# Kernel optimization log

Hardware: AMD Instinct MI355X
Metric: run time of the kernel (lower is better)

## Reference

```python
import jax, jax.numpy as jnp
import numpy as np

B, H0, W0, C = 16, 56, 56, 96
NH, WS, SS = 3, 7, 3
HID, NCL, TAU = 384, 128, 0.5
EPS = 1e-6

def layernorm(x, g, b):
    m = jnp.mean(x, -1, keepdims=True)
    v = jnp.mean((x - m) ** 2, -1, keepdims=True)
    return (x - m) * jax.lax.rsqrt(v + 1e-5) * g + b

def setup_inputs() -> dict:
    key = jax.random.key(0)
    ks = jax.random.split(key, 16)
    s = lambda d: 1.0 / np.sqrt(d)
    return {
        "x": jax.random.normal(ks[0], (B, H0 * W0, C), jnp.float32),
        "norm1_g": jnp.ones((C,)), "norm1_b": jnp.zeros((C,)),
        "qkv_w": jax.random.normal(ks[1], (3 * C, C)) * s(C),
        "qkv_b": jnp.zeros((3 * C,)),
        "proj_w": jax.random.normal(ks[2], (C, C)) * s(C),
        "proj_b": jnp.zeros((C,)),
        "norm2_g": jnp.ones((C,)), "norm2_b": jnp.zeros((C,)),
        "ffn_norm_g": jnp.ones((C,)), "ffn_norm_b": jnp.zeros((C,)),
        "pin_w": jax.random.normal(ks[3], (HID, C)) * s(C),
        "pin_b": jnp.zeros((HID,)),
        "tm_inc": jax.random.normal(ks[4], (NCL, 2 * HID)) * 0.5,
        "tm_out": jax.random.normal(ks[5], (NCL, C)) * s(NCL),
        "gate": jnp.float32(0.5),
        "H": H0, "W": W0,
    }

def window_attention(win, qkv_w, qkv_b, proj_w, proj_b):
    N, T, Cc = win.shape
    hd = Cc // NH
    qkv = win @ qkv_w.T + qkv_b                      # [N, T, 3C]
    qkv = qkv.reshape(N, T, 3, NH, hd).transpose(2, 0, 3, 1, 4)
    q, k, v = qkv[0], qkv[1], qkv[2]                 # [N, nh, T, hd]
    attn = jax.nn.softmax(jnp.einsum('nhqd,nhkd->nhqk', q, k) * (hd ** -0.5), axis=-1)
    out = jnp.einsum('nhqk,nhkd->nhqd', attn, v).transpose(0, 2, 1, 3).reshape(N, T, Cc)
    return out @ proj_w.T + proj_b

def tm_ffn(x, ffn_norm_g, ffn_norm_b, pin_w, pin_b, tm_inc, tm_out, gate):
    # x: [B, T, C]
    Bb, T, Cc = x.shape
    y = jax.nn.sigmoid(layernorm(x, ffn_norm_g, ffn_norm_b) @ pin_w.T + pin_b)  # [B,T,HID]
    flat = y.reshape(Bb * T, HID)
    lits = jnp.clip(jnp.concatenate([flat, 1.0 - flat], axis=-1), EPS, 1.0)     # [N, 2*HID]
    m = jax.nn.sigmoid(tm_inc)
    hard = (m > TAU).astype(m.dtype)
    m_ste = m + jax.lax.stop_gradient(hard - m)      # binary via STE
    # binary mask -> conjunction prod_k l_k^{m_jk} = exp(log(l) @ m^T)
    clauses = jnp.exp(jnp.log(lits) @ m_ste.T)       # [N, NCL]
    logits = (clauses @ tm_out).reshape(Bb, T, Cc)
    g = jax.nn.sigmoid(gate)
    return g * logits + (1.0 - g) * jax.nn.sigmoid(logits)

def reference(x, norm1_g, norm1_b, qkv_w, qkv_b, proj_w, proj_b,
              norm2_g, norm2_b, ffn_norm_g, ffn_norm_b,
              pin_w, pin_b, tm_inc, tm_out, gate, H, W):
    Bb, L, Cc = x.shape
    shortcut = x
    y = layernorm(x, norm1_g, norm1_b).reshape(Bb, H, W, Cc)
    pad_h = (WS - H % WS) % WS
    pad_w = (WS - W % WS) % WS
    if pad_h or pad_w:
        y = jnp.pad(y, ((0, 0), (0, pad_h), (0, pad_w), (0, 0)))
    Hp, Wp = y.shape[1], y.shape[2]
    if SS > 0:
        y = jnp.roll(y, shift=(-SS, -SS), axis=(1, 2))
    # window partition
    y = y.reshape(Bb, Hp // WS, WS, Wp // WS, WS, Cc).transpose(0, 1, 3, 2, 4, 5)
    win = y.reshape(-1, WS * WS, Cc)
    a = window_attention(win, qkv_w, qkv_b, proj_w, proj_b)
    a = a.reshape(Bb, Hp // WS, Wp // WS, WS, WS, Cc)
    if SS > 0:
        a = jnp.roll(a, shift=(SS, SS), axis=(3, 4))
    # window reverse
    a = a.transpose(0, 1, 3, 2, 4, 5).reshape(Bb, Hp, Wp, Cc)
    if pad_h or pad_w:
        a = a[:, :H, :W, :]
    a = a.reshape(Bb, H * W, Cc)
    x1 = shortcut + a
    x2 = x1 + tm_ffn(layernorm(x1, norm2_g, norm2_b),
                     ffn_norm_g, ffn_norm_b, pin_w, pin_b, tm_inc, tm_out, gate)
    return x2
```

## Files before the change

kernel.cpp:

```cpp
#include <hip/hip_runtime.h>

#define NB 16
#define NHH 56
#define NWW 56
#define NC 96
#define NL (NHH*NWW)
#define NTOK (NB*NL)
#define WSZ 7
#define NT 49
#define SSH 3
#define NWIN 1024
#define HDIM 32
#define HID_ 384
#define NCL_ 128
#define NLIT 768
#define EPS_ 1e-6f
#define LOG_EPS -13.815510558f

typedef unsigned short u16;
typedef unsigned int   u32;
typedef __attribute__((ext_vector_type(8))) short short8;
typedef __attribute__((ext_vector_type(4))) float f32x4;

__device__ __forceinline__ float us2f(u16 u) {
  union { u32 u; float f; } x; x.u = ((u32)u) << 16; return x.f;
}
__device__ __forceinline__ u16 f2us(float f) {
  union { float f; u32 u; } x; x.f = f;
  u32 lsb = (x.u >> 16) & 1u;
  return (u16)((x.u + 0x7fffu + lsb) >> 16);
}
__device__ __forceinline__ float sigmoidf_(float x) { return 1.f / (1.f + __expf(-x)); }

__global__ __launch_bounds__(256) void k0_prep(const float* __restrict__ tm_inc,
                                               const float* __restrict__ pin_w,
                                               const float* __restrict__ tm_out,
                                               const float* __restrict__ qkv_w,
                                               const float* __restrict__ proj_w,
                                               u16* __restrict__ maskb,
                                               u16* __restrict__ pinwb,
                                               u16* __restrict__ tmoT,
                                               u16* __restrict__ qkvwb,
                                               u16* __restrict__ projwb) {
  int idx = blockIdx.x * 256 + threadIdx.x;
  if (idx < NCL_ * NLIT) {
    int c = idx / NLIT, q = idx - c * NLIT;
    int j = (q & 1) ? (q >> 1) + HID_ : (q >> 1);
    maskb[idx] = (tm_inc[(size_t)c * NLIT + j] > 0.f) ? (u16)0x3F80 : (u16)0;
  }
  if (idx < HID_ * NC)
    pinwb[idx] = f2us(pin_w[idx]);
  if (idx < NC * NCL_) {
    int c = idx / NCL_, k = idx - c * NCL_;
    tmoT[idx] = f2us(tm_out[(size_t)k * NC + c]);
  }
  if (idx < 3 * NC * NC)
    qkvwb[idx] = f2us(qkv_w[idx]);
  if (idx < NC * NC)
    projwb[idx] = f2us(proj_w[idx]);
}

__global__ __launch_bounds__(256, 4) void k2_attn(const float* __restrict__ x,
                                               const float* __restrict__ n1g,
                                               const float* __restrict__ n1b,
                                               const u16* __restrict__ qkvwb,
                                               const float* __restrict__ qkv_b,
                                               const u16* __restrict__ projwb,
                                               const float* __restrict__ proj_b,
                                               float* __restrict__ x1) {
  __shared__ __align__(16) u16 syb[64 * 104];
  __shared__ __align__(16) u16 sk [64 * 104];
  __shared__ __align__(16) u16 svT[96 * 72];
  const int tid  = threadIdx.x;
  const int wave = tid >> 6;
  const int lane = tid & 63;
  const int l16  = lane & 15;
  const int quad = lane >> 4;
  const int win  = blockIdx.x;
  const int t0   = wave * 16;
  const int bb = win >> 6, wl = win & 63;
  const int hbase = (wl >> 3) * WSZ, wbase = (wl & 7) * WSZ;

  {
    const int t = tid >> 2, s = tid & 3;
    if (t < NT) {
      int hp = hbase + t / WSZ, wp = wbase + t % WSZ;
      int h = hp + SSH; if (h >= NHH) h -= NHH;
      int w = wp + SSH; if (w >= NWW) w -= NWW;
      const float* xp = x + ((size_t)bb * NL + (size_t)h * NWW + w) * NC;
      float4 v[6];
      float sum = 0.f;
      #pragma unroll
      for (int k = 0; k < 6; ++k) {
        v[k] = *reinterpret_cast<const float4*>(xp + s * 4 + k * 16);
        sum += v[k].x + v[k].y + v[k].z + v[k].w;
      }
      sum += __shfl_xor(sum, 1); sum += __shfl_xor(sum, 2);
      float mean = sum * (1.f / 96.f);
      float ssq = 0.f;
      #pragma unroll
      for (int k = 0; k < 6; ++k) {
        float d0 = v[k].x - mean, d1 = v[k].y - mean;
        float d2 = v[k].z - mean, d3 = v[k].w - mean;
        ssq += d0 * d0 + d1 * d1 + d2 * d2 + d3 * d3;
      }
      ssq += __shfl_xor(ssq, 1); ssq += __shfl_xor(ssq, 2);
      float rstd = rsqrtf(ssq * (1.f / 96.f) + 1e-5f);
      #pragma unroll
      for (int k = 0; k < 6; ++k) {
        int c = s * 4 + k * 16;
        const float4 g4 = *reinterpret_cast<const float4*>(n1g + c);
        const float4 b4 = *reinterpret_cast<const float4*>(n1b + c);
        syb[t * 104 + c + 0] = f2us((v[k].x - mean) * rstd * g4.x + b4.x);
        syb[t * 104 + c + 1] = f2us((v[k].y - mean) * rstd * g4.y + b4.y);
        syb[t * 104 + c + 2] = f2us((v[k].z - mean) * rstd * g4.z + b4.z);
        syb[t * 104 + c + 3] = f2us((v[k].w - mean) * rstd * g4.w + b4.w);
      }
    } else {
      #pragma unroll
      for (int k = 0; k < 6; ++k) {
        int c = s * 4 + k * 16;
        syb[t * 104 + c + 0] = 0; syb[t * 104 + c + 1] = 0;
        syb[t * 104 + c + 2] = 0; syb[t * 104 + c + 3] = 0;
      }
    }
  }

  {
    short8 afr[3];
    #pragma unroll
    for (int ks = 0; ks < 3; ++ks)
      afr[ks] = *reinterpret_cast<const short8*>(&syb[(t0 + l16) * 104 + quad * 8 + ks * 32]);
    short8 rb[4][3];
    #pragma unroll
    for (int p = 0; p < 4; ++p)
      #pragma unroll
      for (int ks = 0; ks < 3; ++ks)
        rb[p][ks] = *reinterpret_cast<const short8*>(
            qkvwb + (size_t)(p * 16 + l16) * NC + quad * 8 + ks * 32);
    #pragma unroll
    for (int nt = 0; nt < 18; ++nt) {
      const int n0 = nt * 16;
      const float bias = qkv_b[n0 + l16];
      short8 b0 = rb[nt & 3][0], b1 = rb[nt & 3][1], b2 = rb[nt & 3][2];
      if (nt + 4 < 18) {
        #pragma unroll
        for (int ks = 0; ks < 3; ++ks)
          rb[nt & 3][ks] = *reinterpret_cast<const short8*>(
              qkvwb + (size_t)((nt + 4) * 16 + l16) * NC + quad * 8 + ks * 32);
      }
      f32x4 acc = {0.f, 0.f, 0.f, 0.f};
      acc = __builtin_amdgcn_mfma_f32_16x16x32_bf16(afr[0], b0, acc, 0, 0, 0);
      acc = __builtin_amdgcn_mfma_f32_16x16x32_bf16(afr[1], b1, acc, 0, 0, 0);
      acc = __builtin_amdgcn_mfma_f32_16x16x32_bf16(afr[2], b2, acc, 0, 0, 0);
      const int part = nt / 6;
      const int oc = n0 - part * 96 + l16;
      if (part < 2) {
        u16* dst = (part == 0) ? syb : sk;
        #pragma unroll
        for (int r = 0; r < 4; ++r)
          dst[(t0 + quad * 4 + r) * 104 + oc] = f2us(acc[r] + bias);
      } else {
        #pragma unroll
        for (int r = 0; r < 4; ++r)
          svT[oc * 72 + (t0 + quad * 4 + r)] = f2us(acc[r] + bias);
      }
    }
  }
  __syncthreads();

  u16* spw = sk + wave * 16 * 72;
  const float sscale = 0.17677669529663687f;
  short8 qf[3];
  f32x4 s[3][4];
  #pragma unroll
  for (int h = 0; h < 3; ++h)
    qf[h] = *reinterpret_cast<const short8*>(&syb[(t0 + l16) * 104 + h * HDIM + quad * 8]);
  #pragma unroll
  for (int h = 0; h < 3; ++h) {
    const int d0 = h * HDIM;
    #pragma unroll
    for (int nt = 0; nt < 4; ++nt) {
      short8 kf = *reinterpret_cast<const short8*>(&sk[(nt * 16 + l16) * 104 + d0 + quad * 8]);
      f32x4 a = {0.f, 0.f, 0.f, 0.f};
      s[h][nt] = __builtin_amdgcn_mfma_f32_16x16x32_bf16(qf[h], kf, a, 0, 0, 0);
    }
  }
  __syncthreads();
  #pragma unroll
  for (int h = 0; h < 3; ++h) {
    const int d0 = h * HDIM;
    #pragma unroll
    for (int nt = 0; nt < 4; ++nt)
      #pragma unroll
      for (int r = 0; r < 4; ++r) s[h][nt][r] *= sscale;
    if (l16 >= 1) {
      #pragma unroll
      for (int r = 0; r < 4; ++r) s[h][3][r] = -1e30f;
    }
    #pragma unroll
    for (int r = 0; r < 4; ++r) {
      float m = fmaxf(fmaxf(s[h][0][r], s[h][1][r]), fmaxf(s[h][2][r], s[h][3][r]));
      #pragma unroll
      for (int off = 8; off > 0; off >>= 1) m = fmaxf(m, __shfl_xor(m, off, 16));
      float e0 = __expf(s[h][0][r] - m), e1 = __expf(s[h][1][r] - m);
      float e2 = __expf(s[h][2][r] - m), e3 = __expf(s[h][3][r] - m);
      float sum = e0 + e1 + e2 + e3;
      #pragma unroll
      for (int off = 8; off > 0; off >>= 1) sum += __shfl_xor(sum, off, 16);
      float inv = 1.f / sum;
      const int row = quad * 4 + r;
      spw[row * 72 +      l16] = f2us(e0 * inv);
      spw[row * 72 + 16 + l16] = f2us(e1 * inv);
      spw[row * 72 + 32 + l16] = f2us(e2 * inv);
      spw[row * 72 + 48 + l16] = f2us(e3 * inv);
    }
    short8 pa[2];
    pa[0] = *reinterpret_cast<const short8*>(&spw[l16 * 72 + quad * 8]);
    pa[1] = *reinterpret_cast<const short8*>(&spw[l16 * 72 + 32 + quad * 8]);
    #pragma unroll
    for (int nt = 0; nt < 2; ++nt) {
      const int c0 = d0 + nt * 16;
      f32x4 acc = {0.f, 0.f, 0.f, 0.f};
      #pragma unroll
      for (int ks = 0; ks < 2; ++ks) {
        short8 vb = *reinterpret_cast<const short8*>(&svT[(c0 + l16) * 72 + ks * 32 + quad * 8]);
        acc = __builtin_amdgcn_mfma_f32_16x16x32_bf16(pa[ks], vb, acc, 0, 0, 0);
      }
      #pragma unroll
      for (int r = 0; r < 4; ++r)
        syb[(t0 + quad * 4 + r) * 104 + c0 + l16] = f2us(acc[r]);
    }
  }

  {
    short8 aa[3];
    #pragma unroll
    for (int ks = 0; ks < 3; ++ks)
      aa[ks] = *reinterpret_cast<const short8*>(&syb[(t0 + l16) * 104 + quad * 8 + ks * 32]);

    size_t tokr[4]; bool tval[4];
    #pragma unroll
    for (int r = 0; r < 4; ++r) {
      const int t = t0 + quad * 4 + r;
      tval[r] = (t < NT);
      int rr = t / WSZ + SSH; if (rr >= WSZ) rr -= WSZ;
      int qq = t % WSZ + SSH; if (qq >= WSZ) qq -= WSZ;
      tokr[r] = (size_t)bb * NL + (size_t)(hbase + rr) * NWW + (wbase + qq);
    }
    float xv[6][4];
    #pragma unroll
    for (int nt = 0; nt < 6; ++nt)
      #pragma unroll
      for (int r = 0; r < 4; ++r)
        xv[nt][r] = tval[r] ? x[tokr[r] * NC + nt * 16 + l16] : 0.f;

    short8 pbr[2][3];
    #pragma unroll
    for (int ks = 0; ks < 3; ++ks)
      pbr[0][ks] = *reinterpret_cast<const short8*>(
          projwb + (size_t)l16 * NC + quad * 8 + ks * 32);
    #pragma unroll
    for (int nt = 0; nt < 6; ++nt) {
      const int n0 = nt * 16;
      const float pb = proj_b[n0 + l16];
      short8 b0 = pbr[nt & 1][0], b1 = pbr[nt & 1][1], b2 = pbr[nt & 1][2];
      if (nt + 1 < 6) {
        #pragma unroll
        for (int ks = 0; ks < 3; ++ks)
          pbr[(nt + 1) & 1][ks] = *reinterpret_cast<const short8*>(
              projwb + (size_t)((nt + 1) * 16 + l16) * NC + quad * 8 + ks * 32);
      }
      f32x4 acc = {0.f, 0.f, 0.f, 0.f};
      acc = __builtin_amdgcn_mfma_f32_16x16x32_bf16(aa[0], b0, acc, 0, 0, 0);
      acc = __builtin_amdgcn_mfma_f32_16x16x32_bf16(aa[1], b1, acc, 0, 0, 0);
      acc = __builtin_amdgcn_mfma_f32_16x16x32_bf16(aa[2], b2, acc, 0, 0, 0);
      #pragma unroll
      for (int r = 0; r < 4; ++r) {
        if (tval[r])
          x1[tokr[r] * NC + n0 + l16] = xv[nt][r] + acc[r] + pb;
      }
    }
  }
}

__global__ __launch_bounds__(256, 6) void k4_ffn(const float* __restrict__ x1,
                                              const float* __restrict__ g2,
                                              const float* __restrict__ b2,
                                              const float* __restrict__ gf,
                                              const float* __restrict__ bf,
                                              const u16* __restrict__ pinwb,
                                              const float* __restrict__ pin_b,
                                              const u16* __restrict__ maskb,
                                              const u16* __restrict__ tmoT,
                                              const float* __restrict__ gate,
                                              float* __restrict__ out) {
  __shared__ __align__(16) u16 lit[16 * 776];
  u16* szb  = lit;
  u16* claT = lit;
  const int tid  = threadIdx.x;
  const int wave = tid >> 6;
  const int lane = tid & 63;
  const int l16  = lane & 15;
  const int quad = lane >> 4;
  const size_t tok0 = (size_t)blockIdx.x * 16;

  {
    const int t = tid >> 4, s = tid & 15;
    const float* xp = x1 + (tok0 + t) * NC;
    float2 v[3];
    float sum = 0.f;
    #pragma unroll
    for (int k = 0; k < 3; ++k) {
      const int c = s * 2 + k * 32;
      v[k] = *reinterpret_cast<const float2*>(xp + c);
      sum += v[k].x + v[k].y;
    }
    #pragma unroll
    for (int off = 8; off > 0; off >>= 1) sum += __shfl_xor(sum, off, 16);
    const float mean = sum * (1.f / 96.f);
    float ssq = 0.f;
    #pragma unroll
    for (int k = 0; k < 3; ++k) {
      float d0 = v[k].x - mean, d1 = v[k].y - mean;
      ssq += d0 * d0 + d1 * d1;
    }
    #pragma unroll
    for (int off = 8; off > 0; off >>= 1) ssq += __shfl_xor(ssq, off, 16);
    const float rstd = rsqrtf(ssq * (1.f / 96.f) + 1e-5f);
    float tv[6];
    float sum2 = 0.f;
    #pragma unroll
    for (int k = 0; k < 3; ++k) {
      const int c = s * 2 + k * 32;
      const float2 gg = *reinterpret_cast<const float2*>(g2 + c);
      const float2 bb = *reinterpret_cast<const float2*>(b2 + c);
      tv[2 * k]     = (v[k].x - mean) * rstd * gg.x + bb.x;
      tv[2 * k + 1] = (v[k].y - mean) * rstd * gg.y + bb.y;
      sum2 += tv[2 * k] + tv[2 * k + 1];
    }
    #pragma unroll
    for (int off = 8; off > 0; off >>= 1) sum2 += __shfl_xor(sum2, off, 16);
    const float mean2 = sum2 * (1.f / 96.f);
    float ssq2 = 0.f;
    #pragma unroll
    for (int k = 0; k < 3; ++k) {
      float d0 = tv[2 * k] - mean2, d1 = tv[2 * k + 1] - mean2;
      ssq2 += d0 * d0 + d1 * d1;
    }
    #pragma unroll
    for (int off = 8; off > 0; off >>= 1) ssq2 += __shfl_xor(ssq2, off, 16);
    const float rstd2 = rsqrtf(ssq2 * (1.f / 96.f) + 1e-5f);
    #pragma unroll
    for (int k = 0; k < 3; ++k) {
      const int c = s * 2 + k * 32;
      const float2 gg = *reinterpret_cast<const float2*>(gf + c);
      const float2 bb = *reinterpret_cast<const float2*>(bf + c);
      u16 lo = f2us((tv[2 * k]     - mean2) * rstd2 * gg.x + bb.x);
      u16 hi = f2us((tv[2 * k + 1] - mean2) * rstd2 * gg.y + bb.y);
      *reinterpret_cast<u32*>(&szb[t * 104 + c]) = (u32)lo | ((u32)hi << 16);
    }
  }
  __syncthreads();

  const float gv = sigmoidf_(gate[0]);

  short8 a_pin[3];
  #pragma unroll
  for (int ks = 0; ks < 3; ++ks)
    a_pin[ks] = *reinterpret_cast<const short8*>(
        &szb[l16 * 104 + quad * 8 + ks * 32]);
  __syncthreads();

  {
    short8 pb[2][3];
    #pragma unroll
    for (int p = 0; p < 2; ++p)
      #pragma unroll
      for (int ks = 0; ks < 3; ++ks)
        pb[p][ks] = *reinterpret_cast<const short8*>(
            pinwb + (size_t)((wave * 6 + p) * 16 + l16) * NC + quad * 8 + ks * 32);
    #pragma unroll
    for (int i = 0; i < 6; ++i) {
      const int o = (wave * 6 + i) * 16 + l16;
      const float pbv = pin_b[o];
      short8 b0 = pb[i & 1][0], b1 = pb[i & 1][1], b2 = pb[i & 1][2];
      if (i + 2 < 6) {
        #pragma unroll
        for (int ks = 0; ks < 3; ++ks)
          pb[i & 1][ks] = *reinterpret_cast<const short8*>(
              pinwb + (size_t)((wave * 6 + i + 2) * 16 + l16) * NC + quad * 8 + ks * 32);
      }
      f32x4 acc = {0.f, 0.f, 0.f, 0.f};
      acc = __builtin_amdgcn_mfma_f32_16x16x32_bf16(a_pin[0], b0, acc, 0, 0, 0);
      acc = __builtin_amdgcn_mfma_f32_16x16x32_bf16(a_pin[1], b1, acc, 0, 0, 0);
      acc = __builtin_amdgcn_mfma_f32_16x16x32_bf16(a_pin[2], b2, acc, 0, 0, 0);
      #pragma unroll
      for (int r = 0; r < 4; ++r) {
        const float a0 = acc[r] + pbv;
        const float sp0 = fmaxf(a0, 0.f) + __logf(1.f + __expf(-fabsf(a0)));
        const int ta = quad * 4 + r;
        const u16 lo0 = f2us(fmaxf(a0 - sp0, LOG_EPS));
        const u16 hi0 = f2us(fmaxf(-sp0, LOG_EPS));
        *reinterpret_cast<u32*>(&lit[ta * 776 + 2 * o]) = (u32)lo0 | ((u32)hi0 << 16);
      }
    }
  }
  __syncthreads();

  const int nnt = (wave < 2) ? 2 : 1;
  int ntl[2]; ntl[0] = wave; ntl[1] = wave + 4;
  float xr[2][4];
  #pragma unroll
  for (int j = 0; j < 2; ++j) {
    if (j < nnt) {
      const int c = ntl[j] * 16 + l16;
      #pragma unroll
      for (int r = 0; r < 4; ++r)
        xr[j][r] = x1[(tok0 + quad * 4 + r) * NC + c];
    }
  }

  {
    const int ct0 = 2 * wave;
    const u16* bp0 = maskb + (size_t)(ct0 * 16 + l16) * NLIT + quad * 8;
    const u16* bp1 = maskb + (size_t)((ct0 + 1) * 16 + l16) * NLIT + quad * 8;
    short8 rb0[4], rb1[4];
    #pragma unroll
    for (int p = 0; p < 4; ++p) {
      rb0[p] = *reinterpret_cast<const short8*>(bp0 + p * 32);
      rb1[p] = *reinterpret_cast<const short8*>(bp1 + p * 32);
    }
    f32x4 c0 = {0.f, 0.f, 0.f, 0.f}, c1 = {0.f, 0.f, 0.f, 0.f};
    #pragma unroll
    for (int ks = 0; ks < 24; ++ks) {
      const int k0 = ks * 32 + quad * 8;
      short8 a0 = *reinterpret_cast<const short8*>(&lit[l16 * 776 + k0]);
      short8 b0 = rb0[ks & 3], b1 = rb1[ks & 3];
      if (ks + 4 < 24) {
        rb0[ks & 3] = *reinterpret_cast<const short8*>(bp0 + (ks + 4) * 32);
        rb1[ks & 3] = *reinterpret_cast<const short8*>(bp1 + (ks + 4) * 32);
      }
      c0 = __builtin_amdgcn_mfma_f32_16x16x32_bf16(a0, b0, c0, 0, 0, 0);
      c1 = __builtin_amdgcn_mfma_f32_16x16x32_bf16(a0, b1, c1, 0, 0, 0);
    }
    float e0[4], e1[4];
    #pragma unroll
    for (int r = 0; r < 4; ++r) { e0[r] = __expf(c0[r]); e1[r] = __expf(c1[r]); }
    __syncthreads();
    #pragma unroll
    for (int r = 0; r < 4; ++r) {
      const int ta = quad * 4 + r;
      claT[ta * 136 + ct0 * 16 + l16]        = f2us(e0[r]);
      claT[ta * 136 + (ct0 + 1) * 16 + l16]  = f2us(e1[r]);
    }
  }
  __syncthreads();

  #pragma unroll
  for (int j = 0; j < 2; ++j) {
    if (j < nnt) {
      const int nt = ntl[j];
      short8 btm[4];
      #pragma unroll
      for (int ks = 0; ks < 4; ++ks)
        btm[ks] = *reinterpret_cast<const short8*>(
            tmoT + (size_t)(nt * 16 + l16) * NCL_ + ks * 32 + quad * 8);
      f32x4 acc = {0.f, 0.f, 0.f, 0.f};
      #pragma unroll
      for (int ks = 0; ks < 4; ++ks) {
        const int k0 = ks * 32 + quad * 8;
        short8 a0 = *reinterpret_cast<const short8*>(&claT[l16 * 136 + k0]);
        acc = __builtin_amdgcn_mfma_f32_16x16x32_bf16(a0, btm[ks], acc, 0, 0, 0);
      }
      const int c = nt * 16 + l16;
      #pragma unroll
      for (int r = 0; r < 4; ++r) {
        const int ta = quad * 4 + r;
        float lg = acc[r];
        out[(tok0 + ta) * NC + c] = xr[j][r] + gv * lg + (1.f - gv) * sigmoidf_(lg);
      }
    }
  }
}

extern "C" void kernel_launch(void* const* d_in, const int* in_sizes, int n_in,
                              void* d_out, int out_size, void* d_ws, size_t ws_size,
                              hipStream_t stream) {
  (void)in_sizes; (void)n_in; (void)out_size; (void)ws_size;
  const float* x      = (const float*)d_in[0];
  const float* n1g    = (const float*)d_in[1];
  const float* n1b    = (const float*)d_in[2];
  const float* qkv_w  = (const float*)d_in[3];
  const float* qkv_b  = (const float*)d_in[4];
  const float* proj_w = (const float*)d_in[5];
  const float* proj_b = (const float*)d_in[6];
  const float* n2g    = (const float*)d_in[7];
  const float* n2b    = (const float*)d_in[8];
  const float* fng    = (const float*)d_in[9];
  const float* fnb    = (const float*)d_in[10];
  const float* pin_w  = (const float*)d_in[11];
  const float* pin_b  = (const float*)d_in[12];
  const float* tm_inc = (const float*)d_in[13];
  const float* tm_out = (const float*)d_in[14];
  const float* gate   = (const float*)d_in[15];

  float* x1 = (float*)d_ws;
  u16* maskb = (u16*)(x1 + (size_t)NTOK * NC);
  u16* pinwb = maskb + NCL_ * NLIT;
  u16* tmoT  = pinwb + HID_ * NC;
  u16* qkvwb = tmoT + NC * NCL_;
  u16* projwb= qkvwb + 3 * NC * NC;

  hipLaunchKernelGGL(k0_prep, dim3(384), dim3(256), 0, stream,
                     tm_inc, pin_w, tm_out, qkv_w, proj_w, maskb, pinwb, tmoT, qkvwb, projwb);
  hipLaunchKernelGGL(k2_attn, dim3(NWIN), dim3(256), 0, stream,
                     x, n1g, n1b, qkvwb, qkv_b, projwb, proj_b, x1);
  hipLaunchKernelGGL(k4_ffn, dim3(NTOK / 16), dim3(256), 0, stream,
                     x1, n2g, n2b, fng, fnb, pinwb, pin_b, maskb, tmoT, gate, (float*)d_out);
}
```

Baseline: 226.2 us.

## Fuse pin projection into clause GEMM per wave with register-resident literals

Restructures the FFN kernel so each wave owns 32 tokens. It computes the pin projection in 32-wide hidden chunks and feeds the resulting log-literals straight from MFMA output registers into the clause MFMA, so the large literal matrix is no longer staged through shared memory. The block-wide syncthreads between stages are gone, and each block now covers 128 tokens instead of 16, so the mask and pin weight loads are amortised over more tokens. In exchange the kernel holds many more registers per thread (occupancy hint drops from 6 to 2 blocks), and it relies on the MFMA accumulator layout lining up with the A-operand layout. There are also fewer blocks to spread across the GPU.

```diff
diff --git a/kernel.cpp b/kernel.cpp
--- a/kernel.cpp
+++ b/kernel.cpp
@@ -284,7 +284,58 @@
   }
 }
 
-__global__ __launch_bounds__(256, 6) void k4_ffn(const float* __restrict__ x1,
+__device__ __forceinline__ short8 lit_pack(f32x4 p, f32x4 pbv) {
+  union { short8 s; u32 w[4]; } u;
+  #pragma unroll
+  for (int r = 0; r < 4; ++r) {
+    const float a  = p[r] + pbv[r];
+    const float sp = fmaxf(a, 0.f) + __logf(1.f + __expf(-fabsf(a)));
+    const u16 lo = f2us(fmaxf(a - sp, LOG_EPS));
+    const u16 hi = f2us(fmaxf(-sp,    LOG_EPS));
+    u.w[r] = (u32)lo | ((u32)hi << 16);
+  }
+  return u.s;
+}
+
+__device__ __forceinline__ void k4_step(int ks, bool pref,
+    const u16* __restrict__ pinwb, const float* __restrict__ pin_b,
+    const u16* __restrict__ maskb, int l16, int quad,
+    short8 (&pa)[3], f32x4& pbv, short8 (&mb)[8],
+    const short8 (&zb)[2][3], f32x4 (&cacc)[2][8]) {
+  const short8 a0 = pa[0], a1 = pa[1], a2 = pa[2];
+  const f32x4 pb = pbv;
+  f32x4 p0 = {0.f, 0.f, 0.f, 0.f}, p1 = {0.f, 0.f, 0.f, 0.f};
+  p0 = __builtin_amdgcn_mfma_f32_16x16x32_bf16(a0, zb[0][0], p0, 0, 0, 0);
+  p1 = __builtin_amdgcn_mfma_f32_16x16x32_bf16(a0, zb[1][0], p1, 0, 0, 0);
+  p0 = __builtin_amdgcn_mfma_f32_16x16x32_bf16(a1, zb[0][1], p0, 0, 0, 0);
+  p1 = __builtin_amdgcn_mfma_f32_16x16x32_bf16(a1, zb[1][1], p1, 0, 0, 0);
+  p0 = __builtin_amdgcn_mfma_f32_16x16x32_bf16(a2, zb[0][2], p0, 0, 0, 0);
+  p1 = __builtin_amdgcn_mfma_f32_16x16x32_bf16(a2, zb[1][2], p1, 0, 0, 0);
+  if (pref) {
+    const u16* pp = pinwb + (size_t)((ks + 2) * 16 + l16) * NC + quad * 8;
+    pa[0] = *reinterpret_cast<const short8*>(pp);
+    pa[1] = *reinterpret_cast<const short8*>(pp + 32);
+    pa[2] = *reinterpret_cast<const short8*>(pp + 64);
+    pbv   = *reinterpret_cast<const f32x4*>(pin_b + (ks + 2) * 16 + quad * 4);
+  }
+  const short8 lf0 = lit_pack(p0, pb);
+  const short8 lf1 = lit_pack(p1, pb);
+  #pragma unroll
+  for (int ct = 0; ct < 8; ++ct) {
+    cacc[0][ct] = __builtin_amdgcn_mfma_f32_16x16x32_bf16(lf0, mb[ct], cacc[0][ct], 0, 0, 0);
+    cacc[1][ct] = __builtin_amdgcn_mfma_f32_16x16x32_bf16(lf1, mb[ct], cacc[1][ct], 0, 0, 0);
+  }
+  if (pref) {
+    #pragma unroll
+    for (int ct = 0; ct < 8; ++ct)
+      mb[ct] = *reinterpret_cast<const short8*>(
+          maskb + (size_t)(ct * 16 + l16) * NLIT + (ks + 2) * 32 + quad * 8);
+  }
+}
+
+__device__ __forceinline__ float sum4_(float4 v) { return (v.x + v.y) + (v.z + v.w); }
+
+__global__ __launch_bounds__(256, 2) void k4_ffn(const float* __restrict__ x1,
                                               const float* __restrict__ g2,
                                               const float* __restrict__ b2,
                                               const float* __restrict__ gf,
@@ -295,191 +346,175 @@
                                               const u16* __restrict__ tmoT,
                                               const float* __restrict__ gate,
                                               float* __restrict__ out) {
-  __shared__ __align__(16) u16 lit[16 * 776];
-  u16* szb  = lit;
-  u16* claT = lit;
+  __shared__ __align__(16) u16 claT_s[4 * 32 * 136];
   const int tid  = threadIdx.x;
   const int wave = tid >> 6;
   const int lane = tid & 63;
   const int l16  = lane & 15;
   const int quad = lane >> 4;
-  const size_t tok0 = (size_t)blockIdx.x * 16;
-
-  {
-    const int t = tid >> 4, s = tid & 15;
-    const float* xp = x1 + (tok0 + t) * NC;
-    float2 v[3];
+  u16* claT = claT_s + wave * 32 * 136;
+  const size_t tok0 = (size_t)blockIdx.x * 128 + wave * 32;
+
+  float4 g2v[3][2], b2v[3][2], gfv[3][2], bfv[3][2];
+  #pragma unroll
+  for (int k = 0; k < 3; ++k) {
+    const int c = k * 32 + quad * 8;
+    g2v[k][0] = *reinterpret_cast<const float4*>(g2 + c);
+    g2v[k][1] = *reinterpret_cast<const float4*>(g2 + c + 4);
+    b2v[k][0] = *reinterpret_cast<const float4*>(b2 + c);
+    b2v[k][1] = *reinterpret_cast<const float4*>(b2 + c + 4);
+    gfv[k][0] = *reinterpret_cast<const float4*>(gf + c);
+    gfv[k][1] = *reinterpret_cast<const float4*>(gf + c + 4);
+    bfv[k][0] = *reinterpret_cast<const float4*>(bf + c);
+    bfv[k][1] = *reinterpret_cast<const float4*>(bf + c + 4);
+  }
+  short8 zb[2][3];
+  #pragma unroll
+  for (int g = 0; g < 2; ++g) {
+    const float* xp = x1 + (tok0 + g * 16 + l16) * NC + quad * 8;
+    float4 va[3], vb[3];
     float sum = 0.f;
     #pragma unroll
     for (int k = 0; k < 3; ++k) {
-      const int c = s * 2 + k * 32;
-      v[k] = *reinterpret_cast<const float2*>(xp + c);
-      sum += v[k].x + v[k].y;
-    }
-    #pragma unroll
-    for (int off = 8; off > 0; off >>= 1) sum += __shfl_xor(sum, off, 16);
+      va[k] = *reinterpret_cast<const float4*>(xp + k * 32);
+      vb[k] = *reinterpret_cast<const float4*>(xp + k * 32 + 4);
+      sum += sum4_(va[k]) + sum4_(vb[k]);
+    }
+    sum += __shfl_xor(sum, 16); sum += __shfl_xor(sum, 32);
     const float mean = sum * (1.f / 96.f);
     float ssq = 0.f;
     #pragma unroll
     for (int k = 0; k < 3; ++k) {
-      float d0 = v[k].x - mean, d1 = v[k].y - mean;
-      ssq += d0 * d0 + d1 * d1;
-    }
-    #pragma unroll
-    for (int off = 8; off > 0; off >>= 1) ssq += __shfl_xor(ssq, off, 16);
+      float d;
+      d = va[k].x - mean; ssq += d * d;  d = va[k].y - mean; ssq += d * d;
+      d = va[k].z - mean; ssq += d * d;  d = va[k].w - mean; ssq += d * d;
+      d = vb[k].x - mean; ssq += d * d;  d = vb[k].y - mean; ssq += d * d;
+      d = vb[k].z - mean; ssq += d * d;  d = vb[k].w - mean; ssq += d * d;
+    }
+    ssq += __shfl_xor(ssq, 16); ssq += __shfl_xor(ssq, 32);
     const float rstd = rsqrtf(ssq * (1.f / 96.f) + 1e-5f);
-    float tv[6];
     float sum2 = 0.f;
     #pragma unroll
     for (int k = 0; k < 3; ++k) {
-      const int c = s * 2 + k * 32;
-      const float2 gg = *reinterpret_cast<const float2*>(g2 + c);
-      const float2 bb = *reinterpret_cast<const float2*>(b2 + c);
-      tv[2 * k]     = (v[k].x - mean) * rstd * gg.x + bb.x;
-      tv[2 * k + 1] = (v[k].y - mean) * rstd * gg.y + bb.y;
-      sum2 += tv[2 * k] + tv[2 * k + 1];
-    }
-    #pragma unroll
-    for (int off = 8; off > 0; off >>= 1) sum2 += __shfl_xor(sum2, off, 16);
+      va[k].x = (va[k].x - mean) * rstd * g2v[k][0].x + b2v[k][0].x; sum2 += va[k].x;
+      va[k].y = (va[k].y - mean) * rstd * g2v[k][0].y + b2v[k][0].y; sum2 += va[k].y;
+      va[k].z = (va[k].z - mean) * rstd * g2v[k][0].z + b2v[k][0].z; sum2 += va[k].z;
+      va[k].w = (va[k].w - mean) * rstd * g2v[k][0].w + b2v[k][0].w; sum2 += va[k].w;
+      vb[k].x = (vb[k].x - mean) * rstd * g2v[k][1].x + b2v[k][1].x; sum2 += vb[k].x;
+      vb[k].y = (vb[k].y - mean) * rstd * g2v[k][1].y + b2v[k][1].y; sum2 += vb[k].y;
+      vb[k].z = (vb[k].z - mean) * rstd * g2v[k][1].z + b2v[k][1].z; sum2 += vb[k].z;
+      vb[k].w = (vb[k].w - mean) * rstd * g2v[k][1].w + b2v[k][1].w; sum2 += vb[k].w;
+    }
+    sum2 += __shfl_xor(sum2, 16); sum2 += __shfl_xor(sum2, 32);
     const float mean2 = sum2 * (1.f / 96.f);
     float ssq2 = 0.f;
     #pragma unroll
     for (int k = 0; k < 3; ++k) {
-      float d0 = tv[2 * k] - mean2, d1 = tv[2 * k + 1] - mean2;
-      ssq2 += d0 * d0 + d1 * d1;
-    }
-    #pragma unroll
-    for (int off = 8; off > 0; off >>= 1) ssq2 += __shfl_xor(ssq2, off, 16);
+      float d;
+      d = va[k].x - mean2; ssq2 += d * d;  d = va[k].y - mean2; ssq2 += d * d;
+      d = va[k].z - mean2; ssq2 += d * d;  d = va[k].w - mean2; ssq2 += d * d;
+      d = vb[k].x - mean2; ssq2 += d * d;  d = vb[k].y - mean2; ssq2 += d * d;
+      d = vb[k].z - mean2; ssq2 += d * d;  d = vb[k].w - mean2; ssq2 += d * d;
+    }
+    ssq2 += __shfl_xor(ssq2, 16); ssq2 += __shfl_xor(ssq2, 32);
     const float rstd2 = rsqrtf(ssq2 * (1.f / 96.f) + 1e-5f);
     #pragma unroll
     for (int k = 0; k < 3; ++k) {
-      const int c = s * 2 + k * 32;
-      const float2 gg = *reinterpret_cast<const float2*>(gf + c);
-      const float2 bb = *reinterpret_cast<const float2*>(bf + c);
-      u16 lo = f2us((tv[2 * k]     - mean2) * rstd2 * gg.x + bb.x);
-      u16 hi = f2us((tv[2 * k + 1] - mean2) * rstd2 * gg.y + bb.y);
-      *reinterpret_cast<u32*>(&szb[t * 104 + c]) = (u32)lo | ((u32)hi << 16);
-    }
-  }
-  __syncthreads();
-
+      const float z0 = (va[k].x - mean2) * rstd2 * gfv[k][0].x + bfv[k][0].x;
+      const float z1 = (va[k].y - mean2) * rstd2 * gfv[k][0].y + bfv[k][0].y;
+      const float z2 = (va[k].z - mean2) * rstd2 * gfv[k][0].z + bfv[k][0].z;
+      const float z3 = (va[k].w - mean2) * rstd2 * gfv[k][0].w + bfv[k][0].w;
+      const float z4 = (vb[k].x - mean2) * rstd2 * gfv[k][1].x + bfv[k][1].x;
+      const float z5 = (vb[k].y - mean2) * rstd2 * gfv[k][1].y + bfv[k][1].y;
+      const float z6 = (vb[k].z - mean2) * rstd2 * gfv[k][1].z + bfv[k][1].z;
+      const float z7 = (vb[k].w - mean2) * rstd2 * gfv[k][1].w + bfv[k][1].w;
+      union { short8 s; u32 w[4]; } uz;
+      uz.w[0] = (u32)f2us(z0) | ((u32)f2us(z1) << 16);
+      uz.w[1] = (u32)f2us(z2) | ((u32)f2us(z3) << 16);
+      uz.w[2] = (u32)f2us(z4) | ((u32)f2us(z5) << 16);
+      uz.w[3] = (u32)f2us(z6) | ((u32)f2us(z7) << 16);
+      zb[g][k] = uz.s;
+    }
+  }
+
+  short8 paA[3], paB[3], mbA[8], mbB[8];
+  f32x4 pbvA, pbvB;
+  {
+    const u16* pp0 = pinwb + (size_t)(l16) * NC + quad * 8;
+    const u16* pp1 = pinwb + (size_t)(16 + l16) * NC + quad * 8;
+    #pragma unroll
+    for (int k = 0; k < 3; ++k) {
+      paA[k] = *reinterpret_cast<const short8*>(pp0 + k * 32);
+      paB[k] = *reinterpret_cast<const short8*>(pp1 + k * 32);
+    }
+    pbvA = *reinterpret_cast<const f32x4*>(pin_b + quad * 4);
+    pbvB = *reinterpret_cast<const f32x4*>(pin_b + 16 + quad * 4);
+    #pragma unroll
+    for (int ct = 0; ct < 8; ++ct) {
+      const u16* mp = maskb + (size_t)(ct * 16 + l16) * NLIT + quad * 8;
+      mbA[ct] = *reinterpret_cast<const short8*>(mp);
+      mbB[ct] = *reinterpret_cast<const short8*>(mp + 32);
+    }
+  }
+  f32x4 cacc[2][8];
+  {
+    const f32x4 z4 = {0.f, 0.f, 0.f, 0.f};
+    #pragma unroll
+    for (int g = 0; g < 2; ++g)
+      #pragma unroll
+      for (int ct = 0; ct < 8; ++ct)
+        cacc[g][ct] = z4;
+  }
+
+  for (int kk = 0; kk < 12; ++kk) {
+    k4_step(2 * kk,     kk < 11, pinwb, pin_b, maskb, l16, quad, paA, pbvA, mbA, zb, cacc);
+    k4_step(2 * kk + 1, kk < 11, pinwb, pin_b, maskb, l16, quad, paB, pbvB, mbB, zb, cacc);
+  }
+
+  float xr[2][6][4];
+  #pragma unroll
+  for (int g = 0; g < 2; ++g)
+    #pragma unroll
+    for (int nt = 0; nt < 6; ++nt)
+      #pragma unroll
+      for (int r = 0; r < 4; ++r)
+        xr[g][nt][r] = x1[(tok0 + g * 16 + quad * 4 + r) * NC + nt * 16 + l16];
+
+  #pragma unroll
+  for (int g = 0; g < 2; ++g)
+    #pragma unroll
+    for (int ct = 0; ct < 8; ++ct)
+      #pragma unroll
+      for (int r = 0; r < 4; ++r)
+        claT[(g * 16 + quad * 4 + r) * 136 + ct * 16 + l16] = f2us(__expf(cacc[g][ct][r]));
+
+  short8 caf[2][4];
+  #pragma unroll
+  for (int g = 0; g < 2; ++g)
+    #pragma unroll
+    for (int ks = 0; ks < 4; ++ks)
+      caf[g][ks] = *reinterpret_cast<const short8*>(
+          &claT[(g * 16 + l16) * 136 + ks * 32 + quad * 8]);
   const float gv = sigmoidf_(gate[0]);
-
-  short8 a_pin[3];
-  #pragma unroll
-  for (int ks = 0; ks < 3; ++ks)
-    a_pin[ks] = *reinterpret_cast<const short8*>(
-        &szb[l16 * 104 + quad * 8 + ks * 32]);
-  __syncthreads();
-
-  {
-    short8 pb[2][3];
-    #pragma unroll
-    for (int p = 0; p < 2; ++p)
-      #pragma unroll
-      for (int ks = 0; ks < 3; ++ks)
-        pb[p][ks] = *reinterpret_cast<const short8*>(
-            pinwb + (size_t)((wave * 6 + p) * 16 + l16) * NC + quad * 8 + ks * 32);
-    #pragma unroll
-    for (int i = 0; i < 6; ++i) {
-      const int o = (wave * 6 + i) * 16 + l16;
-      const float pbv = pin_b[o];
-      short8 b0 = pb[i & 1][0], b1 = pb[i & 1][1], b2 = pb[i & 1][2];
-      if (i + 2 < 6) {
-        #pragma unroll
-        for (int ks = 0; ks < 3; ++ks)
-          pb[i & 1][ks] = *reinterpret_cast<const short8*>(
-              pinwb + (size_t)((wave * 6 + i + 2) * 16 + l16) * NC + quad * 8 + ks * 32);
-      }
-      f32x4 acc = {0.f, 0.f, 0.f, 0.f};
-      acc = __builtin_amdgcn_mfma_f32_16x16x32_bf16(a_pin[0], b0, acc, 0, 0, 0);
-      acc = __builtin_amdgcn_mfma_f32_16x16x32_bf16(a_pin[1], b1, acc, 0, 0, 0);
-      acc = __builtin_amdgcn_mfma_f32_16x16x32_bf16(a_pin[2], b2, acc, 0, 0, 0);
-      #pragma unroll
-      for (int r = 0; r < 4; ++r) {
-        const float a0 = acc[r] + pbv;
-        const float sp0 = fmaxf(a0, 0.f) + __logf(1.f + __expf(-fabsf(a0)));
-        const int ta = quad * 4 + r;
-        const u16 lo0 = f2us(fmaxf(a0 - sp0, LOG_EPS));
-        const u16 hi0 = f2us(fmaxf(-sp0, LOG_EPS));
-        *reinterpret_cast<u32*>(&lit[ta * 776 + 2 * o]) = (u32)lo0 | ((u32)hi0 << 16);
-      }
-    }
-  }
-  __syncthreads();
-
-  const int nnt = (wave < 2) ? 2 : 1;
-  int ntl[2]; ntl[0] = wave; ntl[1] = wave + 4;
-  float xr[2][4];
-  #pragma unroll
-  for (int j = 0; j < 2; ++j) {
-    if (j < nnt) {
-      const int c = ntl[j] * 16 + l16;
-      #pragma unroll
-      for (int r = 0; r < 4; ++r)
-        xr[j][r] = x1[(tok0 + quad * 4 + r) * NC + c];
-    }
-  }
-
-  {
-    const int ct0 = 2 * wave;
-    const u16* bp0 = maskb + (size_t)(ct0 * 16 + l16) * NLIT + quad * 8;
-    const u16* bp1 = maskb + (size_t)((ct0 + 1) * 16 + l16) * NLIT + quad * 8;
-    short8 rb0[4], rb1[4];
-    #pragma unroll
-    for (int p = 0; p < 4; ++p) {
-      rb0[p] = *reinterpret_cast<const short8*>(bp0 + p * 32);
-      rb1[p] = *reinterpret_cast<const short8*>(bp1 + p * 32);
-    }
-    f32x4 c0 = {0.f, 0.f, 0.f, 0.f}, c1 = {0.f, 0.f, 0.f, 0.f};
-    #pragma unroll
-    for (int ks = 0; ks < 24; ++ks) {
-      const int k0 = ks * 32 + quad * 8;
-      short8 a0 = *reinterpret_cast<const short8*>(&lit[l16 * 776 + k0]);
-      short8 b0 = rb0[ks & 3], b1 = rb1[ks & 3];
-      if (ks + 4 < 24) {
-        rb0[ks & 3] = *reinterpret_cast<const short8*>(bp0 + (ks + 4) * 32);
-        rb1[ks & 3] = *reinterpret_cast<const short8*>(bp1 + (ks + 4) * 32);
-      }
-      c0 = __builtin_amdgcn_mfma_f32_16x16x32_bf16(a0, b0, c0, 0, 0, 0);
-      c1 = __builtin_amdgcn_mfma_f32_16x16x32_bf16(a0, b1, c1, 0, 0, 0);
-    }
-    float e0[4], e1[4];
-    #pragma unroll
-    for (int r = 0; r < 4; ++r) { e0[r] = __expf(c0[r]); e1[r] = __expf(c1[r]); }
-    __syncthreads();
+  #pragma unroll
+  for (int nt = 0; nt < 6; ++nt) {
+    short8 btm[4];
+    #pragma unroll
+    for (int ks = 0; ks < 4; ++ks)
+      btm[ks] = *reinterpret_cast<const short8*>(
+          tmoT + (size_t)(nt * 16 + l16) * NCL_ + ks * 32 + quad * 8);
+    f32x4 o0 = {0.f, 0.f, 0.f, 0.f}, o1 = {0.f, 0.f, 0.f, 0.f};
+    #pragma unroll
+    for (int ks = 0; ks < 4; ++ks) {
+      o0 = __builtin_amdgcn_mfma_f32_16x16x32_bf16(caf[0][ks], btm[ks], o0, 0, 0, 0);
+      o1 = __builtin_amdgcn_mfma_f32_16x16x32_bf16(caf[1][ks], btm[ks], o1, 0, 0, 0);
+    }
+    const int c = nt * 16 + l16;
     #pragma unroll
     for (int r = 0; r < 4; ++r) {
-      const int ta = quad * 4 + r;
-      claT[ta * 136 + ct0 * 16 + l16]        = f2us(e0[r]);
-      claT[ta * 136 + (ct0 + 1) * 16 + l16]  = f2us(e1[r]);
-    }
-  }
-  __syncthreads();
-
-  #pragma unroll
-  for (int j = 0; j < 2; ++j) {
-    if (j < nnt) {
-      const int nt = ntl[j];
-      short8 btm[4];
-      #pragma unroll
-      for (int ks = 0; ks < 4; ++ks)
-        btm[ks] = *reinterpret_cast<const short8*>(
-            tmoT + (size_t)(nt * 16 + l16) * NCL_ + ks * 32 + quad * 8);
-      f32x4 acc = {0.f, 0.f, 0.f, 0.f};
-      #pragma unroll
-      for (int ks = 0; ks < 4; ++ks) {
-        const int k0 = ks * 32 + quad * 8;
-        short8 a0 = *reinterpret_cast<const short8*>(&claT[l16 * 136 + k0]);
-        acc = __builtin_amdgcn_mfma_f32_16x16x32_bf16(a0, btm[ks], acc, 0, 0, 0);
-      }
-      const int c = nt * 16 + l16;
-      #pragma unroll
-      for (int r = 0; r < 4; ++r) {
-        const int ta = quad * 4 + r;
-        float lg = acc[r];
-        out[(tok0 + ta) * NC + c] = xr[j][r] + gv * lg + (1.f - gv) * sigmoidf_(lg);
-      }
+      const float lg0 = o0[r], lg1 = o1[r];
+      out[(tok0 + quad * 4 + r) * NC + c]      = xr[0][nt][r] + gv * lg0 + (1.f - gv) * sigmoidf_(lg0);
+      out[(tok0 + 16 + quad * 4 + r) * NC + c] = xr[1][nt][r] + gv * lg1 + (1.f - gv) * sigmoidf_(lg1);
     }
   }
 }
@@ -516,6 +551,6 @@
                      tm_inc, pin_w, tm_out, qkv_w, proj_w, maskb, pinwb, tmoT, qkvwb, projwb);
   hipLaunchKernelGGL(k2_attn, dim3(NWIN), dim3(256), 0, stream,
                      x, n1g, n1b, qkvwb, qkv_b, projwb, proj_b, x1);
-  hipLaunchKernelGGL(k4_ffn, dim3(NTOK / 16), dim3(256), 0, stream,
+  hipLaunchKernelGGL(k4_ffn, dim3(NTOK / 128), dim3(256), 0, stream,
                      x1, n2g, n2b, fng, fnb, pinwb, pin_b, maskb, tmoT, gate, (float*)d_out);
 }
```

After: 196.5 us. -13.1%, faster.
